# Optimization experiments

Hardware: AMD Instinct MI355X
Metric: run time of the kernel (lower is better)

## Reference

```python
import jax, jax.numpy as jnp
import numpy as np

EMBED_DIM = 1024
NUM_HEADS = 16
HEAD_DIM = EMBED_DIM // NUM_HEADS
ROPE_BASE = 10000.0


def _rope_cos_sin(seq_len, head_dim, dtype):
    # Standard RoPE (ESM-style rotate_half): freqs outer(t, inv_freq), emb = cat(freqs, freqs)
    inv_freq = 1.0 / (ROPE_BASE ** (jnp.arange(0, head_dim, 2, dtype=jnp.float32) / head_dim))
    t = jnp.arange(seq_len, dtype=jnp.float32)
    freqs = jnp.einsum('s,d->sd', t, inv_freq)          # [s, d/2]
    emb = jnp.concatenate([freqs, freqs], axis=-1)      # [s, d]
    return jnp.cos(emb).astype(dtype), jnp.sin(emb).astype(dtype)


def _rotate_half(x):
    x1, x2 = jnp.split(x, 2, axis=-1)
    return jnp.concatenate([-x2, x1], axis=-1)


def _apply_rope(x, cos, sin):
    # x: [b, h, s, d]; cos/sin: [s, d] broadcast over b, h
    return x * cos + _rotate_half(x) * sin


def setup_inputs() -> dict:
    key = jax.random.key(0)
    ks = jax.random.split(key, 5)
    b, s, e = 4, 2048, EMBED_DIM
    scale = 1.0 / np.sqrt(e)
    x = jax.random.normal(ks[0], (b, s, e), dtype=jnp.float32)
    Wqkv = jax.random.normal(ks[1], (e, 3 * e), dtype=jnp.float32) * scale
    bqkv = jnp.zeros((3 * e,), dtype=jnp.float32)
    Wo = jax.random.normal(ks[2], (e, e), dtype=jnp.float32) * scale
    bo = jnp.zeros((e,), dtype=jnp.float32)
    return {"x": x, "Wqkv": Wqkv, "bqkv": bqkv, "Wo": Wo, "bo": bo}


def reference(x, Wqkv, bqkv, Wo, bo):
    b, s, e = x.shape
    h, d = NUM_HEADS, HEAD_DIM
    qkv = jnp.einsum('bse,ef->bsf', x, Wqkv) + bqkv          # [b, s, 3e]
    q, k, v = jnp.split(qkv, 3, axis=-1)
    # b s (h d) -> b h s d
    q = q.reshape(b, s, h, d).transpose(0, 2, 1, 3)
    k = k.reshape(b, s, h, d).transpose(0, 2, 1, 3)
    v = v.reshape(b, s, h, d).transpose(0, 2, 1, 3)
    cos, sin = _rope_cos_sin(s, d, x.dtype)
    q = _apply_rope(q, cos, sin)
    k = _apply_rope(k, cos, sin)
    # scaled dot product attention (no mask, no dropout, non-causal)
    scores = jnp.einsum('bhqd,bhkd->bhqk', q, k) / jnp.asarray(np.sqrt(d), x.dtype)
    attn = jax.nn.softmax(scores, axis=-1)
    out = jnp.einsum('bhqk,bhkd->bhqd', attn, v)             # [b, h, s, d]
    out = out.transpose(0, 2, 1, 3).reshape(b, s, e)         # b h s d -> b s (h d)
    return jnp.einsum('bse,ef->bsf', out, Wo) + bo
```

## Files before the change

### kernel.cpp

```cpp
#include <hip/hip_runtime.h>
#include <stdint.h>
#include <stddef.h>

typedef __bf16 bf16;
typedef __attribute__((ext_vector_type(8))) __bf16 bf16x8;
typedef __attribute__((ext_vector_type(4))) __bf16 bf16x4;
typedef __attribute__((ext_vector_type(4))) float f32x4;
typedef __attribute__((ext_vector_type(4))) float float4v;

#define BATCH 4
#define SEQ   2048
#define EMB   1024
#define NH    16
#define HD    64
#define F3    3072

#define MFMA16(a, b, c) __builtin_amdgcn_mfma_f32_16x16x32_bf16((a), (b), (c), 0, 0, 0)

__device__ __forceinline__ void gload_lds16(const bf16* g, bf16* l) {
  __builtin_amdgcn_global_load_lds(
      (const __attribute__((address_space(1))) uint32_t*)g,
      (__attribute__((address_space(3))) uint32_t*)l, 16, 0, 0);
}

__global__ __launch_bounds__(256) void rope_table(float* __restrict__ cosT,
                                                  float* __restrict__ sinT) {
  int idx = blockIdx.x * 256 + threadIdx.x;
  int pos = idx >> 5, d1 = idx & 31;
  float inv = powf(10000.0f, -(float)(2 * d1) / 64.0f);
  float th = (float)pos * inv;
  cosT[idx] = cosf(th);
  sinT[idx] = sinf(th);
}

__global__ __launch_bounds__(256) void convert_bf16(const float* __restrict__ src,
                                                    bf16* __restrict__ dst, int n4) {
  int i = blockIdx.x * 256 + threadIdx.x;
  if (i >= n4) return;
  float4v v = ((const float4v*)src)[i];
  bf16x4 o;
#pragma unroll
  for (int k = 0; k < 4; ++k) o[k] = (bf16)v[k];
  ((bf16x4*)dst)[i] = o;
}

__global__ __launch_bounds__(256) void transpose_f32_bf16(const float* __restrict__ in,
                                                          bf16* __restrict__ out,
                                                          int R, int C) {
  __shared__ bf16 tile[32][33];
  const int tx = threadIdx.x & 31;
  const int ty = threadIdx.x >> 5;
  const int c0 = blockIdx.x * 32, r0 = blockIdx.y * 32;
#pragma unroll
  for (int kk = 0; kk < 4; ++kk) {
    int r = ty + kk * 8;
    tile[r][tx] = (bf16)in[(size_t)(r0 + r) * C + c0 + tx];
  }
  __syncthreads();
#pragma unroll
  for (int kk = 0; kk < 4; ++kk) {
    int r = ty + kk * 8;
    out[(size_t)(c0 + r) * R + r0 + tx] = tile[tx][r];
  }
}

__global__ __launch_bounds__(256) void qkv_rope_kernel(
    const bf16* __restrict__ x, const bf16* __restrict__ wT,
    const float* __restrict__ bias, bf16* __restrict__ qo, bf16* __restrict__ ko,
    bf16* __restrict__ vo, const float* __restrict__ cosT,
    const float* __restrict__ sinT) {
  __shared__ __align__(16) bf16 As[128 * 32];
  __shared__ __align__(16) bf16 Bs[128 * 32];
  const int tid = threadIdx.x;
  const int w = tid >> 6, lane = tid & 63;
  const int lhi = lane >> 4, llo = lane & 15;
  const int wr = w >> 1, wc = w & 1;
  const int row_a0 = blockIdx.y * 128;
  const int row_b0 = blockIdx.x * 128;

  f32x4 acc[4][4];
#pragma unroll
  for (int i = 0; i < 4; ++i)
#pragma unroll
    for (int j = 0; j < 4; ++j) acc[i][j] = (f32x4){0.f, 0.f, 0.f, 0.f};

  for (int k0 = 0; k0 < EMB; k0 += 32) {
#pragma unroll
    for (int c = 0; c < 2; ++c) {
      int chunk = w * 2 + c;
      int gl = chunk * 64 + lane;
      int row = gl >> 2, kk = (gl & 3) << 3;
      gload_lds16(x + (size_t)(row_a0 + row) * EMB + k0 + kk, &As[chunk * 512]);
      gload_lds16(wT + (size_t)(row_b0 + row) * EMB + k0 + kk, &Bs[chunk * 512]);
    }
    __syncthreads();
    bf16x8 a[4], b[4];
#pragma unroll
    for (int i = 0; i < 4; ++i)
      a[i] = *(const bf16x8*)&As[(wr * 64 + i * 16 + llo) * 32 + lhi * 8];
#pragma unroll
    for (int j = 0; j < 4; ++j)
      b[j] = *(const bf16x8*)&Bs[(wc * 64 + j * 16 + llo) * 32 + lhi * 8];
#pragma unroll
    for (int i = 0; i < 4; ++i)
#pragma unroll
      for (int j = 0; j < 4; ++j) acc[i][j] = MFMA16(a[i], b[j], acc[i][j]);
    __syncthreads();
  }

  const int f0 = row_b0 + wc * 64;
  const int part = f0 >> 10;
  const int hh = (f0 & 1023) >> 6;
  const int m_base = row_a0 + wr * 64;

  float bvals[4];
#pragma unroll
  for (int j = 0; j < 4; ++j) bvals[j] = bias[f0 + j * 16 + llo];

  if (part == 2) {
#pragma unroll
    for (int i = 0; i < 4; ++i) {
      int m0 = m_base + i * 16 + lhi * 4;
      int bb = m0 >> 11, pos0 = m0 & 2047;
#pragma unroll
      for (int j = 0; j < 4; ++j) {
        int dd = j * 16 + llo;
        bf16x4 pk;
#pragma unroll
        for (int r = 0; r < 4; ++r) pk[r] = (bf16)(acc[i][j][r] + bvals[j]);
        *(bf16x4*)(vo + ((size_t)(bb * NH + hh) * HD + dd) * SEQ + pos0) = pk;
      }
    }
  } else {
    bf16* dst = (part == 0) ? qo : ko;
    const float qs = (part == 0) ? 0.125f : 1.0f;
#pragma unroll
    for (int i = 0; i < 4; ++i) {
#pragma unroll
      for (int r = 0; r < 4; ++r) {
        int m = m_base + i * 16 + lhi * 4 + r;
        int bb = m >> 11, pos = m & 2047;
        size_t base = ((size_t)(bb * NH + hh) * SEQ + pos) * HD;
#pragma unroll
        for (int j = 0; j < 2; ++j) {
          int d1 = j * 16 + llo;
          float x1 = acc[i][j][r] + bvals[j];
          float x2 = acc[i][j + 2][r] + bvals[j + 2];
          float cth = cosT[pos * 32 + d1];
          float sth = sinT[pos * 32 + d1];
          dst[base + d1] = (bf16)((x1 * cth - x2 * sth) * qs);
          dst[base + d1 + 32] = (bf16)((x2 * cth + x1 * sth) * qs);
        }
      }
    }
  }
}

__global__ __launch_bounds__(512) void attn_kernel(const bf16* __restrict__ q,
                                                   const bf16* __restrict__ k,
                                                   const bf16* __restrict__ vT,
                                                   bf16* __restrict__ o) {
  __shared__ __align__(16) bf16 smem[32768];
  bf16* Qs = smem;

  const int tid = threadIdx.x, w = tid >> 6, lane = tid & 63;
  const int lhi = lane >> 4, llo = lane & 15;
  const int l7 = llo & 7;
  const int bidx = blockIdx.x;
  const int vblk = (bidx & 7) * 64 + (bidx >> 3);
  const int qt = vblk & 7, bh = vblk >> 3;
  const bf16* qbase = q + (size_t)bh * SEQ * HD + qt * 256 * HD;
  const bf16* kbase = k + (size_t)bh * SEQ * HD;
  const bf16* vbase = vT + (size_t)bh * HD * SEQ;
  bf16* Pw = smem + w * 2048;

  const int rowc = lane >> 3;
  const int sw8 = (lane & 7) ^ rowc;

#pragma unroll
  for (int c = 0; c < 4; ++c) {
    int chunk = w * 4 + c;
    int row = chunk * 8 + rowc;
    gload_lds16(qbase + (size_t)row * HD + sw8 * 8, &Qs[chunk * 512]);
  }
  if (w < 4) {
#pragma unroll
    for (int c = 0; c < 2; ++c) {
      int chunk = w * 2 + c;
      int row = chunk * 8 + rowc;
      gload_lds16(kbase + (size_t)row * HD + sw8 * 8, &smem[16384 + chunk * 512]);
    }
  } else {
#pragma unroll
    for (int c = 0; c < 2; ++c) {
      int chunk = (w - 4) * 2 + c;
      int row = chunk * 8 + rowc;
      gload_lds16(vbase + (size_t)row * SEQ + sw8 * 8, &smem[24576 + chunk * 512]);
    }
  }
  __syncthreads();

  bf16x8 qf[2][2];
#pragma unroll
  for (int i = 0; i < 2; ++i)
#pragma unroll
    for (int kc = 0; kc < 2; ++kc)
      qf[i][kc] = *(const bf16x8*)&Qs[(w * 32 + i * 16 + llo) * 64 +
                                      (((kc * 4 + lhi) ^ l7) * 8)];
  __syncthreads();

  float rsum[2] = {0.f, 0.f};
  f32x4 oacc[2][4];
#pragma unroll
  for (int i = 0; i < 2; ++i)
#pragma unroll
    for (int j = 0; j < 4; ++j) oacc[i][j] = (f32x4){0.f, 0.f, 0.f, 0.f};

  for (int kb = 0; kb < 32; ++kb) {
    bf16* Kc = smem + 16384 + (kb & 1) * 4096;
    bf16* Vc = smem + 24576 + (kb & 1) * 4096;
    if (kb < 31) {
      int kpos = (kb + 1) * 64;
      if (w < 4) {
        bf16* Kn = smem + 16384 + ((kb + 1) & 1) * 4096;
#pragma unroll
        for (int c = 0; c < 2; ++c) {
          int chunk = w * 2 + c;
          int row = chunk * 8 + rowc;
          gload_lds16(kbase + (size_t)(kpos + row) * HD + sw8 * 8, &Kn[chunk * 512]);
        }
      } else {
        bf16* Vn = smem + 24576 + ((kb + 1) & 1) * 4096;
#pragma unroll
        for (int c = 0; c < 2; ++c) {
          int chunk = (w - 4) * 2 + c;
          int row = chunk * 8 + rowc;
          gload_lds16(vbase + (size_t)row * SEQ + kpos + sw8 * 8, &Vn[chunk * 512]);
        }
      }
    }
    f32x4 st[4][2];
#pragma unroll
    for (int tt = 0; tt < 4; ++tt)
#pragma unroll
      for (int i = 0; i < 2; ++i) st[tt][i] = (f32x4){0.f, 0.f, 0.f, 0.f};
#pragma unroll
    for (int kc = 0; kc < 2; ++kc) {
      bf16x8 kfr[4];
#pragma unroll
      for (int tt = 0; tt < 4; ++tt)
        kfr[tt] = *(const bf16x8*)&Kc[(tt * 16 + llo) * 64 +
                                      (((kc * 4 + lhi) ^ l7) * 8)];
#pragma unroll
      for (int tt = 0; tt < 4; ++tt)
#pragma unroll
        for (int i = 0; i < 2; ++i)
          st[tt][i] = MFMA16(kfr[tt], qf[i][kc], st[tt][i]);
    }
#pragma unroll
    for (int tt = 0; tt < 4; ++tt) {
#pragma unroll
      for (int i = 0; i < 2; ++i) {
        bf16x4 pk;
        float a = 0.f;
#pragma unroll
        for (int r = 0; r < 4; ++r) {
          float p = __expf(st[tt][i][r]);
          pk[r] = (bf16)p;
          a += p;
        }
        rsum[i] += a;
        int gi = (tt * 4 + lhi) ^ (l7 << 1);
        *(bf16x4*)&Pw[(i * 16 + llo) * 64 + gi * 4] = pk;
      }
    }
#pragma unroll
    for (int kc = 0; kc < 2; ++kc) {
      bf16x8 af[2], bv[4];
      int xg = ((kc * 4 + lhi) ^ l7) * 8;
      int pg = ((kc * 8 + lhi * 2) ^ (l7 << 1)) * 4;
#pragma unroll
      for (int i = 0; i < 2; ++i)
        af[i] = *(const bf16x8*)&Pw[(i * 16 + llo) * 64 + pg];
#pragma unroll
      for (int jd = 0; jd < 4; ++jd)
        bv[jd] = *(const bf16x8*)&Vc[(jd * 16 + llo) * 64 + xg];
#pragma unroll
      for (int i = 0; i < 2; ++i)
#pragma unroll
        for (int jd = 0; jd < 4; ++jd) oacc[i][jd] = MFMA16(af[i], bv[jd], oacc[i][jd]);
    }
    __syncthreads();
  }

  const int bb = bh >> 4, hh = bh & 15;
#pragma unroll
  for (int i = 0; i < 2; ++i) {
    float t = rsum[i];
    t += __shfl_xor(t, 16);
    t += __shfl_xor(t, 32);
#pragma unroll
    for (int r = 0; r < 4; ++r) {
      float l = __shfl(t, lhi * 4 + r);
      float inv = 1.0f / l;
      int pos = qt * 256 + w * 32 + i * 16 + lhi * 4 + r;
      size_t base = ((size_t)bb * SEQ + pos) * EMB + hh * HD;
#pragma unroll
      for (int jd = 0; jd < 4; ++jd)
        o[base + jd * 16 + llo] = (bf16)(oacc[i][jd][r] * inv);
    }
  }
}

__global__ __launch_bounds__(256) void outproj_kernel(const bf16* __restrict__ a_in,
                                                      const bf16* __restrict__ wT,
                                                      const float* __restrict__ bo,
                                                      float* __restrict__ out) {
  __shared__ __align__(16) bf16 As[128 * 32];
  __shared__ __align__(16) bf16 Bs[128 * 32];
  const int tid = threadIdx.x;
  const int w = tid >> 6, lane = tid & 63;
  const int lhi = lane >> 4, llo = lane & 15;
  const int wr = w >> 1, wc = w & 1;
  const int row_a0 = blockIdx.y * 128;
  const int row_b0 = blockIdx.x * 128;

  f32x4 acc[4][4];
#pragma unroll
  for (int i = 0; i < 4; ++i)
#pragma unroll
    for (int j = 0; j < 4; ++j) acc[i][j] = (f32x4){0.f, 0.f, 0.f, 0.f};

  for (int k0 = 0; k0 < EMB; k0 += 32) {
#pragma unroll
    for (int c = 0; c < 2; ++c) {
      int chunk = w * 2 + c;
      int gl = chunk * 64 + lane;
      int row = gl >> 2, kk = (gl & 3) << 3;
      gload_lds16(a_in + (size_t)(row_a0 + row) * EMB + k0 + kk, &As[chunk * 512]);
      gload_lds16(wT + (size_t)(row_b0 + row) * EMB + k0 + kk, &Bs[chunk * 512]);
    }
    __syncthreads();
    bf16x8 a[4], b[4];
#pragma unroll
    for (int i = 0; i < 4; ++i)
      a[i] = *(const bf16x8*)&As[(wr * 64 + i * 16 + llo) * 32 + lhi * 8];
#pragma unroll
    for (int j = 0; j < 4; ++j)
      b[j] = *(const bf16x8*)&Bs[(wc * 64 + j * 16 + llo) * 32 + lhi * 8];
#pragma unroll
    for (int i = 0; i < 4; ++i)
#pragma unroll
      for (int j = 0; j < 4; ++j) acc[i][j] = MFMA16(a[i], b[j], acc[i][j]);
    __syncthreads();
  }

  const int col0 = row_b0 + wc * 64;
  const int m_base = row_a0 + wr * 64;
  float bvals[4];
#pragma unroll
  for (int j = 0; j < 4; ++j) bvals[j] = bo[col0 + j * 16 + llo];
#pragma unroll
  for (int i = 0; i < 4; ++i) {
#pragma unroll
    for (int r = 0; r < 4; ++r) {
      int m = m_base + i * 16 + lhi * 4 + r;
#pragma unroll
      for (int j = 0; j < 4; ++j)
        out[(size_t)m * EMB + col0 + j * 16 + llo] = acc[i][j][r] + bvals[j];
    }
  }
}

extern "C" void kernel_launch(void* const* d_in, const int* in_sizes, int n_in,
                              void* d_out, int out_size, void* d_ws, size_t ws_size,
                              hipStream_t stream) {
  const float* x_raw = (const float*)d_in[0];
  const float* wqkv_raw = (const float*)d_in[1];
  const float* bqkv = (const float*)d_in[2];
  const float* wo_raw = (const float*)d_in[3];
  const float* bo = (const float*)d_in[4];
  float* out = (float*)d_out;

  char* ws = (char*)d_ws;
  bf16* qw = (bf16*)(ws);
  bf16* kw = (bf16*)(ws + 16777216);
  bf16* vw = (bf16*)(ws + 33554432);
  bf16* wqkvT = (bf16*)(ws + 50331648);
  float* cosT = (float*)(ws + 56623104);
  float* sinT = (float*)(ws + 56885248);
  bf16* ow = (bf16*)(ws + 50331648);
  bf16* woT = (bf16*)(ws);
  bf16* xb = (bf16*)d_out;

  rope_table<<<256, 256, 0, stream>>>(cosT, sinT);
  convert_bf16<<<(BATCH * SEQ * EMB / 4 + 255) / 256, 256, 0, stream>>>(
      x_raw, xb, BATCH * SEQ * EMB / 4);
  transpose_f32_bf16<<<dim3(F3 / 32, EMB / 32), 256, 0, stream>>>(wqkv_raw, wqkvT, EMB, F3);

  qkv_rope_kernel<<<dim3(F3 / 128, (BATCH * SEQ) / 128), 256, 0, stream>>>(
      xb, wqkvT, bqkv, qw, kw, vw, cosT, sinT);
  attn_kernel<<<dim3(BATCH * NH * (SEQ / 256)), 512, 0, stream>>>(qw, kw, vw, ow);

  transpose_f32_bf16<<<dim3(EMB / 32, EMB / 32), 256, 0, stream>>>(wo_raw, woT, EMB, EMB);
  outproj_kernel<<<dim3(EMB / 128, (BATCH * SEQ) / 128), 256, 0, stream>>>(
      ow, woT, bo, out);
}
```

Before: 289.6 us.

## Replace QKV and out-proj GEMMs with 256x256 multi-stage pipelined 8-wave core

Both projection GEMMs now share a 256x256-tile, 512-thread core that uses a 10-slot ring buffer in 160KB of dynamic LDS, XOR-swizzled LDS layout, and interleaved global-to-LDS prefetch with MFMA phases guarded by barriers and setprio. It also remaps block indices for L2 locality. The goal is to raise arithmetic intensity and hide load latency compared with the old single-buffered 128x128 tiles, at the cost of fewer blocks, especially for out-proj (128 blocks), and heavy hand-written synchronisation.

```diff
diff --git a/kernel.cpp b/kernel.cpp
--- a/kernel.cpp
+++ b/kernel.cpp
@@ -22,6 +22,8 @@
       (const __attribute__((address_space(1))) uint32_t*)g,
       (__attribute__((address_space(3))) uint32_t*)l, 16, 0, 0);
 }
+
+__device__ __forceinline__ int mod10(int x) { return x >= 10 ? x - 10 : x; }
 
 __global__ __launch_bounds__(256) void rope_table(float* __restrict__ cosT,
                                                   float* __restrict__ sinT) {
@@ -64,54 +66,169 @@
   }
 }
 
-__global__ __launch_bounds__(256) void qkv_rope_kernel(
+__device__ __forceinline__ void gemm256_core(bf16* lds,
+                                             const bf16* __restrict__ Abase,
+                                             const bf16* __restrict__ Bbase,
+                                             f32x4 (&acc)[8][4]) {
+  const int tid = threadIdx.x;
+  const int w = tid >> 6, lane = tid & 63;
+  const int lhi = lane >> 4, llo = lane & 15, l7 = llo & 7;
+  const int wr = w >> 2, wc = w & 3;
+  const int srow = lane >> 3;
+  const int sk16 = (lane & 7) ^ srow;
+  const size_t g_lane = (size_t)(w * 16 + srow) * EMB + sk16 * 8;
+  bf16* ldsw = lds + w * 1024;
+
+  const int ka0 = (lhi * 8) ^ (l7 << 3);
+  const int ka1 = (32 + lhi * 8) ^ (l7 << 3);
+  const int arow = llo * 64;
+  const int brow = ((wc & 1) * 64 + llo) * 64;
+
+#pragma unroll
+  for (int i = 0; i < 8; ++i)
+#pragma unroll
+    for (int j = 0; j < 4; ++j) acc[i][j] = (f32x4){0.f, 0.f, 0.f, 0.f};
+
+#define STAGE(baseptr, slot)                              \
+  do {                                                    \
+    const bf16* _b = (baseptr);                           \
+    bf16* _l = ldsw + (slot) * 8192;                      \
+    gload_lds16(_b + g_lane, _l);                         \
+    gload_lds16(_b + g_lane + 8 * EMB, _l + 512);         \
+  } while (0)
+
+  STAGE(Abase, 0);
+  STAGE(Abase + 128 * EMB, 1);
+  STAGE(Bbase, 2);
+  STAGE(Bbase + 128 * EMB, 3);
+  STAGE(Abase + 64, 4);
+  STAGE(Abase + 128 * EMB + 64, 5);
+  asm volatile("s_waitcnt vmcnt(4)" ::: "memory");
+  __builtin_amdgcn_s_barrier();
+
+  int rs = 0;
+#pragma unroll 1
+  for (int t = 0; t < 16; ++t) {
+    const bf16* ldsA = lds + mod10(rs + wr) * 8192 + arow;
+    const bf16* ldsB = lds + mod10(rs + 2 + (wc >> 1)) * 8192 + brow;
+    const int k1 = (t + 1) * 64;
+    const int k2 = (t + 2) * 64;
+    bf16x8 a[4][2], b0[2][2], b1[2][2];
+
+#pragma unroll
+    for (int i = 0; i < 4; ++i) {
+      a[i][0] = *(const bf16x8*)(ldsA + i * 1024 + ka0);
+      a[i][1] = *(const bf16x8*)(ldsA + i * 1024 + ka1);
+    }
+#pragma unroll
+    for (int j = 0; j < 2; ++j) {
+      b0[j][0] = *(const bf16x8*)(ldsB + j * 1024 + ka0);
+      b0[j][1] = *(const bf16x8*)(ldsB + j * 1024 + ka1);
+    }
+    if (t < 15) STAGE(Bbase + k1, mod10(rs + 6));
+    __builtin_amdgcn_s_barrier();
+    asm volatile("s_waitcnt lgkmcnt(0)" ::: "memory");
+    __builtin_amdgcn_sched_barrier(0);
+    __builtin_amdgcn_s_setprio(1);
+#pragma unroll
+    for (int i = 0; i < 4; ++i)
+#pragma unroll
+      for (int j = 0; j < 2; ++j) {
+        acc[i][j] = MFMA16(a[i][0], b0[j][0], acc[i][j]);
+        acc[i][j] = MFMA16(a[i][1], b0[j][1], acc[i][j]);
+      }
+    __builtin_amdgcn_s_setprio(0);
+    __builtin_amdgcn_s_barrier();
+
+#pragma unroll
+    for (int j = 0; j < 2; ++j) {
+      b1[j][0] = *(const bf16x8*)(ldsB + 2048 + j * 1024 + ka0);
+      b1[j][1] = *(const bf16x8*)(ldsB + 2048 + j * 1024 + ka1);
+    }
+    if (t < 15) STAGE(Bbase + 128 * EMB + k1, mod10(rs + 7));
+    __builtin_amdgcn_s_barrier();
+    asm volatile("s_waitcnt lgkmcnt(0)" ::: "memory");
+    __builtin_amdgcn_sched_barrier(0);
+    __builtin_amdgcn_s_setprio(1);
+#pragma unroll
+    for (int i = 0; i < 4; ++i)
+#pragma unroll
+      for (int j = 0; j < 2; ++j) {
+        acc[i][2 + j] = MFMA16(a[i][0], b1[j][0], acc[i][2 + j]);
+        acc[i][2 + j] = MFMA16(a[i][1], b1[j][1], acc[i][2 + j]);
+      }
+    __builtin_amdgcn_s_setprio(0);
+    __builtin_amdgcn_s_barrier();
+
+#pragma unroll
+    for (int i = 0; i < 4; ++i) {
+      a[i][0] = *(const bf16x8*)(ldsA + 4096 + i * 1024 + ka0);
+      a[i][1] = *(const bf16x8*)(ldsA + 4096 + i * 1024 + ka1);
+    }
+    if (t < 14) STAGE(Abase + k2, mod10(rs + 8));
+    __builtin_amdgcn_s_barrier();
+    asm volatile("s_waitcnt lgkmcnt(0)" ::: "memory");
+    __builtin_amdgcn_sched_barrier(0);
+    __builtin_amdgcn_s_setprio(1);
+#pragma unroll
+    for (int i = 0; i < 4; ++i)
+#pragma unroll
+      for (int j = 0; j < 2; ++j) {
+        acc[4 + i][2 + j] = MFMA16(a[i][0], b1[j][0], acc[4 + i][2 + j]);
+        acc[4 + i][2 + j] = MFMA16(a[i][1], b1[j][1], acc[4 + i][2 + j]);
+      }
+    __builtin_amdgcn_s_setprio(0);
+    __builtin_amdgcn_s_barrier();
+
+    if (t < 14) STAGE(Abase + 128 * EMB + k2, mod10(rs + 9));
+    __builtin_amdgcn_s_barrier();
+    asm volatile("s_waitcnt lgkmcnt(0)" ::: "memory");
+    __builtin_amdgcn_sched_barrier(0);
+    __builtin_amdgcn_s_setprio(1);
+#pragma unroll
+    for (int i = 0; i < 4; ++i)
+#pragma unroll
+      for (int j = 0; j < 2; ++j) {
+        acc[4 + i][j] = MFMA16(a[i][0], b0[j][0], acc[4 + i][j]);
+        acc[4 + i][j] = MFMA16(a[i][1], b0[j][1], acc[4 + i][j]);
+      }
+    __builtin_amdgcn_s_setprio(0);
+    if (t < 14) {
+      asm volatile("s_waitcnt vmcnt(4)" ::: "memory");
+    } else if (t == 14) {
+      asm volatile("s_waitcnt vmcnt(0)" ::: "memory");
+    }
+    if (t < 15) __builtin_amdgcn_s_barrier();
+
+    rs += 4;
+    if (rs >= 10) rs -= 10;
+  }
+#undef STAGE
+}
+
+__global__ __launch_bounds__(512, 2) void qkv8_kernel(
     const bf16* __restrict__ x, const bf16* __restrict__ wT,
     const float* __restrict__ bias, bf16* __restrict__ qo, bf16* __restrict__ ko,
     bf16* __restrict__ vo, const float* __restrict__ cosT,
     const float* __restrict__ sinT) {
-  __shared__ __align__(16) bf16 As[128 * 32];
-  __shared__ __align__(16) bf16 Bs[128 * 32];
+  extern __shared__ __align__(16) bf16 ldsb[];
+  const int orig = blockIdx.x;
+  const int wg = (orig & 7) * 48 + (orig >> 3);
+  const int bx = wg % 12, by = wg / 12;
+  const int row_a0 = by * 256, row_b0 = bx * 256;
+
+  f32x4 acc[8][4];
+  gemm256_core(ldsb, x + (size_t)row_a0 * EMB, wT + (size_t)row_b0 * EMB, acc);
+
   const int tid = threadIdx.x;
   const int w = tid >> 6, lane = tid & 63;
   const int lhi = lane >> 4, llo = lane & 15;
-  const int wr = w >> 1, wc = w & 1;
-  const int row_a0 = blockIdx.y * 128;
-  const int row_b0 = blockIdx.x * 128;
-
-  f32x4 acc[4][4];
-#pragma unroll
-  for (int i = 0; i < 4; ++i)
-#pragma unroll
-    for (int j = 0; j < 4; ++j) acc[i][j] = (f32x4){0.f, 0.f, 0.f, 0.f};
-
-  for (int k0 = 0; k0 < EMB; k0 += 32) {
-#pragma unroll
-    for (int c = 0; c < 2; ++c) {
-      int chunk = w * 2 + c;
-      int gl = chunk * 64 + lane;
-      int row = gl >> 2, kk = (gl & 3) << 3;
-      gload_lds16(x + (size_t)(row_a0 + row) * EMB + k0 + kk, &As[chunk * 512]);
-      gload_lds16(wT + (size_t)(row_b0 + row) * EMB + k0 + kk, &Bs[chunk * 512]);
-    }
-    __syncthreads();
-    bf16x8 a[4], b[4];
-#pragma unroll
-    for (int i = 0; i < 4; ++i)
-      a[i] = *(const bf16x8*)&As[(wr * 64 + i * 16 + llo) * 32 + lhi * 8];
-#pragma unroll
-    for (int j = 0; j < 4; ++j)
-      b[j] = *(const bf16x8*)&Bs[(wc * 64 + j * 16 + llo) * 32 + lhi * 8];
-#pragma unroll
-    for (int i = 0; i < 4; ++i)
-#pragma unroll
-      for (int j = 0; j < 4; ++j) acc[i][j] = MFMA16(a[i], b[j], acc[i][j]);
-    __syncthreads();
-  }
+  const int wr = w >> 2, wc = w & 3;
 
   const int f0 = row_b0 + wc * 64;
   const int part = f0 >> 10;
   const int hh = (f0 & 1023) >> 6;
-  const int m_base = row_a0 + wr * 64;
+  const int m_base = row_a0 + wr * 128;
 
   float bvals[4];
 #pragma unroll
@@ -119,15 +236,15 @@
 
   if (part == 2) {
 #pragma unroll
-    for (int i = 0; i < 4; ++i) {
-      int m0 = m_base + i * 16 + lhi * 4;
+    for (int mi = 0; mi < 8; ++mi) {
+      int m0 = m_base + mi * 16 + lhi * 4;
       int bb = m0 >> 11, pos0 = m0 & 2047;
 #pragma unroll
       for (int j = 0; j < 4; ++j) {
         int dd = j * 16 + llo;
         bf16x4 pk;
 #pragma unroll
-        for (int r = 0; r < 4; ++r) pk[r] = (bf16)(acc[i][j][r] + bvals[j]);
+        for (int r = 0; r < 4; ++r) pk[r] = (bf16)(acc[mi][j][r] + bvals[j]);
         *(bf16x4*)(vo + ((size_t)(bb * NH + hh) * HD + dd) * SEQ + pos0) = pk;
       }
     }
@@ -135,23 +252,57 @@
     bf16* dst = (part == 0) ? qo : ko;
     const float qs = (part == 0) ? 0.125f : 1.0f;
 #pragma unroll
-    for (int i = 0; i < 4; ++i) {
+    for (int mi = 0; mi < 8; ++mi) {
 #pragma unroll
       for (int r = 0; r < 4; ++r) {
-        int m = m_base + i * 16 + lhi * 4 + r;
+        int m = m_base + mi * 16 + lhi * 4 + r;
         int bb = m >> 11, pos = m & 2047;
         size_t base = ((size_t)(bb * NH + hh) * SEQ + pos) * HD;
 #pragma unroll
         for (int j = 0; j < 2; ++j) {
           int d1 = j * 16 + llo;
-          float x1 = acc[i][j][r] + bvals[j];
-          float x2 = acc[i][j + 2][r] + bvals[j + 2];
+          float x1 = acc[mi][j][r] + bvals[j];
+          float x2 = acc[mi][j + 2][r] + bvals[j + 2];
           float cth = cosT[pos * 32 + d1];
           float sth = sinT[pos * 32 + d1];
           dst[base + d1] = (bf16)((x1 * cth - x2 * sth) * qs);
           dst[base + d1 + 32] = (bf16)((x2 * cth + x1 * sth) * qs);
         }
       }
+    }
+  }
+}
+
+__global__ __launch_bounds__(512, 2) void outproj8_kernel(
+    const bf16* __restrict__ a_in, const bf16* __restrict__ wT,
+    const float* __restrict__ bo, float* __restrict__ out) {
+  extern __shared__ __align__(16) bf16 ldsb[];
+  const int orig = blockIdx.x;
+  const int wg = (orig & 7) * 16 + (orig >> 3);
+  const int bx = wg % 4, by = wg / 4;
+  const int row_a0 = by * 256, row_b0 = bx * 256;
+
+  f32x4 acc[8][4];
+  gemm256_core(ldsb, a_in + (size_t)row_a0 * EMB, wT + (size_t)row_b0 * EMB, acc);
+
+  const int tid = threadIdx.x;
+  const int w = tid >> 6, lane = tid & 63;
+  const int lhi = lane >> 4, llo = lane & 15;
+  const int wr = w >> 2, wc = w & 3;
+
+  const int col0 = row_b0 + wc * 64;
+  const int m_base = row_a0 + wr * 128;
+  float bvals[4];
+#pragma unroll
+  for (int j = 0; j < 4; ++j) bvals[j] = bo[col0 + j * 16 + llo];
+#pragma unroll
+  for (int mi = 0; mi < 8; ++mi) {
+#pragma unroll
+    for (int r = 0; r < 4; ++r) {
+      int m = m_base + mi * 16 + lhi * 4 + r;
+#pragma unroll
+      for (int j = 0; j < 4; ++j)
+        out[(size_t)m * EMB + col0 + j * 16 + llo] = acc[mi][j][r] + bvals[j];
     }
   }
 }
@@ -312,66 +463,6 @@
   }
 }
 
-__global__ __launch_bounds__(256) void outproj_kernel(const bf16* __restrict__ a_in,
-                                                      const bf16* __restrict__ wT,
-                                                      const float* __restrict__ bo,
-                                                      float* __restrict__ out) {
-  __shared__ __align__(16) bf16 As[128 * 32];
-  __shared__ __align__(16) bf16 Bs[128 * 32];
-  const int tid = threadIdx.x;
-  const int w = tid >> 6, lane = tid & 63;
-  const int lhi = lane >> 4, llo = lane & 15;
-  const int wr = w >> 1, wc = w & 1;
-  const int row_a0 = blockIdx.y * 128;
-  const int row_b0 = blockIdx.x * 128;
-
-  f32x4 acc[4][4];
-#pragma unroll
-  for (int i = 0; i < 4; ++i)
-#pragma unroll
-    for (int j = 0; j < 4; ++j) acc[i][j] = (f32x4){0.f, 0.f, 0.f, 0.f};
-
-  for (int k0 = 0; k0 < EMB; k0 += 32) {
-#pragma unroll
-    for (int c = 0; c < 2; ++c) {
-      int chunk = w * 2 + c;
-      int gl = chunk * 64 + lane;
-      int row = gl >> 2, kk = (gl & 3) << 3;
-      gload_lds16(a_in + (size_t)(row_a0 + row) * EMB + k0 + kk, &As[chunk * 512]);
-      gload_lds16(wT + (size_t)(row_b0 + row) * EMB + k0 + kk, &Bs[chunk * 512]);
-    }
-    __syncthreads();
-    bf16x8 a[4], b[4];
-#pragma unroll
-    for (int i = 0; i < 4; ++i)
-      a[i] = *(const bf16x8*)&As[(wr * 64 + i * 16 + llo) * 32 + lhi * 8];
-#pragma unroll
-    for (int j = 0; j < 4; ++j)
-      b[j] = *(const bf16x8*)&Bs[(wc * 64 + j * 16 + llo) * 32 + lhi * 8];
-#pragma unroll
-    for (int i = 0; i < 4; ++i)
-#pragma unroll
-      for (int j = 0; j < 4; ++j) acc[i][j] = MFMA16(a[i], b[j], acc[i][j]);
-    __syncthreads();
-  }
-
-  const int col0 = row_b0 + wc * 64;
-  const int m_base = row_a0 + wr * 64;
-  float bvals[4];
-#pragma unroll
-  for (int j = 0; j < 4; ++j) bvals[j] = bo[col0 + j * 16 + llo];
-#pragma unroll
-  for (int i = 0; i < 4; ++i) {
-#pragma unroll
-    for (int r = 0; r < 4; ++r) {
-      int m = m_base + i * 16 + lhi * 4 + r;
-#pragma unroll
-      for (int j = 0; j < 4; ++j)
-        out[(size_t)m * EMB + col0 + j * 16 + llo] = acc[i][j][r] + bvals[j];
-    }
-  }
-}
-
 extern "C" void kernel_launch(void* const* d_in, const int* in_sizes, int n_in,
                               void* d_out, int out_size, void* d_ws, size_t ws_size,
                               hipStream_t stream) {
@@ -393,16 +484,25 @@
   bf16* woT = (bf16*)(ws);
   bf16* xb = (bf16*)d_out;
 
+  static bool attr_set = false;
+  if (!attr_set) {
+    (void)hipFuncSetAttribute((const void*)qkv8_kernel,
+                              hipFuncAttributeMaxDynamicSharedMemorySize, 163840);
+    (void)hipFuncSetAttribute((const void*)outproj8_kernel,
+                              hipFuncAttributeMaxDynamicSharedMemorySize, 163840);
+    attr_set = true;
+  }
+
   rope_table<<<256, 256, 0, stream>>>(cosT, sinT);
   convert_bf16<<<(BATCH * SEQ * EMB / 4 + 255) / 256, 256, 0, stream>>>(
       x_raw, xb, BATCH * SEQ * EMB / 4);
   transpose_f32_bf16<<<dim3(F3 / 32, EMB / 32), 256, 0, stream>>>(wqkv_raw, wqkvT, EMB, F3);
 
-  qkv_rope_kernel<<<dim3(F3 / 128, (BATCH * SEQ) / 128), 256, 0, stream>>>(
+  qkv8_kernel<<<dim3((BATCH * SEQ / 256) * (F3 / 256)), 512, 163840, stream>>>(
       xb, wqkvT, bqkv, qw, kw, vw, cosT, sinT);
   attn_kernel<<<dim3(BATCH * NH * (SEQ / 256)), 512, 0, stream>>>(qw, kw, vw, ow);
 
   transpose_f32_bf16<<<dim3(EMB / 32, EMB / 32), 256, 0, stream>>>(wo_raw, woT, EMB, EMB);
-  outproj_kernel<<<dim3(EMB / 128, (BATCH * SEQ) / 128), 256, 0, stream>>>(
+  outproj8_kernel<<<dim3((BATCH * SEQ / 256) * (EMB / 256)), 512, 163840, stream>>>(
       ow, woT, bo, out);
 }
```

After: 290.7 us. No clear change (+0.4%).
